# Kernel optimization log

Hardware: AMD Instinct MI355X
Metric: run time of the kernel (lower is better)

The kernel has to match this reference:

```python
import jax, jax.numpy as jnp
import numpy as np

N = 20000          # num_nodes
E = 160000         # directed edges (doubled to undirected inside reference)
NF, EF, H, OUT, K = 16, 16, 128, 16, 3


def mlp2(x, w1, b1, w2, b2):
    return jnp.maximum(x @ w1 + b1, 0.0) @ w2 + b2


def edge_agg(x, src, dst, eattr, w1, b1, w2, b2):
    # message = MLP(cat[x_i (target), x_j (source), edge_attr]); aggr='add' at target
    m = mlp2(jnp.concatenate([x[dst], x[src], eattr], axis=-1), w1, b1, w2, b2)
    return jax.ops.segment_sum(m, dst, num_segments=x.shape[0])


def tag_conv(x, src, dst, lins, bias):
    # PyG TAGConv: gcn_norm (no self loops), out = sum_k lin_k(L^k x) + bias
    n = x.shape[0]
    deg = jax.ops.segment_sum(jnp.ones_like(src, dtype=x.dtype), dst, num_segments=n)
    dis = jnp.where(deg > 0, jax.lax.rsqrt(deg), 0.0)
    norm = dis[src] * dis[dst]                     # [E]
    out = x @ lins[0]
    h = x
    for k in range(1, lins.shape[0]):
        h = jax.ops.segment_sum(norm[:, None] * h[src], dst, num_segments=n)
        out = out + h @ lins[k]
    return out + bias


def setup_inputs() -> dict:
    key = jax.random.key(0)
    ks = jax.random.split(key, 20)
    s = 0.05
    lin = lambda k, i, o: jax.random.normal(k, (i, o), jnp.float32) * s
    inp = {}
    inp["x"] = jax.random.normal(ks[0], (N, NF), jnp.float32)
    inp["mask"] = (jax.random.uniform(ks[1], (N, NF)) > 0.5).astype(jnp.float32)
    inp["edge_attr"] = jax.random.normal(ks[2], (E, EF), jnp.float32)
    inp["edge_index"] = jax.random.randint(ks[3], (2, E), 0, N)
    inp["m_w1"] = lin(ks[4], NF, H); inp["m_b1"] = jnp.zeros(H)
    inp["m_w2"] = lin(ks[5], H, NF); inp["m_b2"] = jnp.zeros(NF)
    inp["ea0_w1"] = lin(ks[6], 2 * NF + EF, H); inp["ea0_b1"] = jnp.zeros(H)
    inp["ea0_w2"] = lin(ks[7], H, H); inp["ea0_b2"] = jnp.zeros(H)
    inp["tag0_w"] = jax.random.normal(ks[8], (K + 1, H, H), jnp.float32) * s
    inp["tag0_b"] = jnp.zeros(H)
    inp["ea1_w1"] = lin(ks[9], 2 * H + EF, H); inp["ea1_b1"] = jnp.zeros(H)
    inp["ea1_w2"] = lin(ks[10], H, H); inp["ea1_b2"] = jnp.zeros(H)
    inp["tag1_w"] = jax.random.normal(ks[11], (K + 1, H, H), jnp.float32) * s
    inp["tag1_b"] = jnp.zeros(H)
    inp["ea2_w1"] = lin(ks[12], 2 * H + EF, H); inp["ea2_b1"] = jnp.zeros(H)
    inp["ea2_w2"] = lin(ks[13], H, OUT); inp["ea2_b2"] = jnp.zeros(OUT)
    return inp


def reference(x, mask, edge_attr, m_w1, m_b1, m_w2, m_b2,
              ea0_w1, ea0_b1, ea0_w2, ea0_b2, tag0_w, tag0_b,
              ea1_w1, ea1_b1, ea1_w2, ea1_b2, tag1_w, tag1_b,
              ea2_w1, ea2_b1, ea2_w2, ea2_b2, edge_index):
    # undirect_graph: random directed edges -> duplicate reversed copies
    src0, dst0 = edge_index[0], edge_index[1]
    src = jnp.concatenate([src0, dst0])
    dst = jnp.concatenate([dst0, src0])
    ea = jnp.concatenate([edge_attr, edge_attr], axis=0)
    # mask embedding + residual
    h = mlp2(mask, m_w1, m_b1, m_w2, m_b2) + x
    # [EA, TAG, EA, TAG] with ReLU (dropout = identity in eval)
    h = jnp.maximum(edge_agg(h, src, dst, ea, ea0_w1, ea0_b1, ea0_w2, ea0_b2), 0.0)
    h = jnp.maximum(tag_conv(h, src, dst, tag0_w, tag0_b), 0.0)
    h = jnp.maximum(edge_agg(h, src, dst, ea, ea1_w1, ea1_b1, ea1_w2, ea1_b2), 0.0)
    h = jnp.maximum(tag_conv(h, src, dst, tag1_w, tag1_b), 0.0)
    # final EA (no activation)
    return edge_agg(h, src, dst, ea, ea2_w1, ea2_b1, ea2_w2, ea2_b2)
```

## Files before the change

kernel.cpp:

```cpp
#include <hip/hip_runtime.h>

typedef unsigned short u16;
typedef unsigned int u32;

using bfrag  = __attribute__((ext_vector_type(8))) short;
using f32x4  = __attribute__((ext_vector_type(4))) float;
using f32x16 = __attribute__((ext_vector_type(16))) float;

__device__ __forceinline__ float b2f(u16 u) {
  union { u32 i; float f; } c; c.i = ((u32)u) << 16; return c.f;
}
__device__ __forceinline__ float bflo(u32 u) { union { u32 i; float f; } c; c.i = u << 16; return c.f; }
__device__ __forceinline__ float bfhi(u32 u) { union { u32 i; float f; } c; c.i = u & 0xffff0000u; return c.f; }
__device__ __forceinline__ u16 f2b(float f) {
  union { float f; u32 i; } c; c.f = f;
  u32 x = c.i;
  u32 r = x + 0x7fffu + ((x >> 16) & 1u);
  return (u16)(r >> 16);
}
__device__ __forceinline__ u32 packb2(float x, float y) {
  return ((u32)f2b(x)) | (((u32)f2b(y)) << 16);
}
__device__ __forceinline__ u16 f2h(float x) {
  union { _Float16 h; u16 u; } c; c.h = (_Float16)x; return c.u;
}
__device__ __forceinline__ float h2lo(u32 u) { union { u32 i; _Float16 h[2]; } c; c.i = u; return (float)c.h[0]; }
__device__ __forceinline__ float h2hi(u32 u) { union { u32 i; _Float16 h[2]; } c; c.i = u; return (float)c.h[1]; }
__device__ __forceinline__ int rfl(int v) { return __builtin_amdgcn_readfirstlane(v); }

__global__ __launch_bounds__(256) void prologue(
    const float* __restrict__ ea, const int* __restrict__ eidx,
    const float* __restrict__ ea0_w1, const float* __restrict__ ea0_w2,
    const float* __restrict__ tag0_w, const float* __restrict__ ea1_w1,
    const float* __restrict__ ea1_w2, const float* __restrict__ tag1_w,
    const float* __restrict__ ea2_w1,
    u16* __restrict__ P0, u16* __restrict__ P1, u16* __restrict__ P2,
    int* __restrict__ degi, u16* __restrict__ Wt, int E, int N,
    int PB, int CB) {
  int t = threadIdx.x;
  if (blockIdx.x < (unsigned)PB) {
    __shared__ u16 Alds[64 * 16];
    __shared__ u16 Wlds[3 * 2048];
    int base = blockIdx.x * 64;
    int rows = E - base; if (rows > 64) rows = 64;
    const float* wsrc[3] = { ea0_w1 + 32 * 128, ea1_w1 + 256 * 128, ea2_w1 + 256 * 128 };
#pragma unroll
    for (int i = 0; i < 8; ++i) {
      int idx = i * 256 + t;
      int n = idx >> 4, k = idx & 15;
      Wlds[0 * 2048 + idx] = f2b(wsrc[0][k * 128 + n]);
      Wlds[1 * 2048 + idx] = f2b(wsrc[1][k * 128 + n]);
      Wlds[2 * 2048 + idx] = f2b(wsrc[2][k * 128 + n]);
    }
#pragma unroll
    for (int i = 0; i < 4; ++i) {
      int idx = (i * 256 + t) * 4;
      float4 v = make_float4(0.f, 0.f, 0.f, 0.f);
      if ((idx >> 4) < rows) v = *(const float4*)(ea + (size_t)base * 16 + idx);
      ushort4 h;
      h.x = f2b(v.x); h.y = f2b(v.y); h.z = f2b(v.z); h.w = f2b(v.w);
      *(ushort4*)(Alds + idx) = h;
    }
    __syncthreads();
    int wave = t >> 6, lane = t & 63;
    int rowt = (wave >> 1) * 32;
    int colt = (wave & 1) * 64;
    int mm = lane & 31, kh = lane >> 5;
    bfrag a = *(const bfrag*)(Alds + (rowt + mm) * 16 + kh * 8);
#pragma unroll
    for (int tab = 0; tab < 3; ++tab) {
      const u16* wl = Wlds + tab * 2048;
      bfrag b0 = *(const bfrag*)(wl + (colt + 2 * mm) * 16 + kh * 8);
      bfrag b1 = *(const bfrag*)(wl + (colt + 2 * mm + 1) * 16 + kh * 8);
      f32x16 acc0, acc1;
#pragma unroll
      for (int z = 0; z < 16; ++z) { acc0[z] = 0.f; acc1[z] = 0.f; }
      acc0 = __builtin_amdgcn_mfma_f32_32x32x16_bf16(a, b0, acc0, 0, 0, 0);
      acc1 = __builtin_amdgcn_mfma_f32_32x32x16_bf16(a, b1, acc1, 0, 0, 0);
      u16* P = (tab == 0) ? P0 : (tab == 1) ? P1 : P2;
#pragma unroll
      for (int reg = 0; reg < 16; ++reg) {
        int row = rowt + (reg & 3) + 8 * (reg >> 2) + 4 * kh;
        if (row < rows) {
          u32 pr = ((u32)f2h(acc0[reg])) | (((u32)f2h(acc1[reg])) << 16);
          *(u32*)(P + (size_t)(base + row) * 128 + colt + 2 * mm) = pr;
        }
      }
    }
    return;
  }
  if (blockIdx.x < (unsigned)(PB + CB)) {
    int e = (blockIdx.x - PB) * 256 + t;
    if (e < E) {
      atomicAdd(&degi[eidx[E + e]], 1);
      atomicAdd(&degi[eidx[e]], 1);
    }
    return;
  }
  int wb = blockIdx.x - PB - CB;
  int mat = wb >> 3, chunk = wb & 7;
  const float* src;
  if      (mat == 0)  src = ea0_w2;
  else if (mat <= 4)  src = tag0_w + (mat - 1) * 16384;
  else if (mat == 5)  src = ea1_w1;
  else if (mat == 6)  src = ea1_w1 + 16384;
  else if (mat == 7)  src = ea1_w2;
  else if (mat <= 11) src = tag1_w + (mat - 8) * 16384;
  else if (mat == 12) src = ea2_w1;
  else                src = ea2_w1 + 16384;
  u16* dst = Wt + mat * 16384;
  for (int i = 0; i < 8; ++i) {
    int idx = chunk * 2048 + i * 256 + t;
    int k = idx >> 7, n = idx & 127;
    dst[n * 128 + k] = f2b(src[idx]);
  }
}

__global__ __launch_bounds__(256) void scan1(const int* __restrict__ degi,
                                             int* __restrict__ bsum, int N) {
  __shared__ int sh[256];
  int t = threadIdx.x;
  int gid = blockIdx.x * 256 + t;
  sh[t] = (gid < N) ? degi[gid] : 0;
  __syncthreads();
  for (int off = 128; off > 0; off >>= 1) {
    if (t < off) sh[t] += sh[t + off];
    __syncthreads();
  }
  if (t == 0) bsum[blockIdx.x] = sh[0];
}

__global__ __launch_bounds__(256) void scan2(int* __restrict__ bsum,
                                             int* __restrict__ rowptr, int nb, int N) {
  __shared__ int sh[256];
  int t = threadIdx.x;
  int v = (t < nb) ? bsum[t] : 0;
  sh[t] = v;
  __syncthreads();
  for (int off = 1; off < 256; off <<= 1) {
    int x = sh[t];
    int add = (t >= off) ? sh[t - off] : 0;
    __syncthreads();
    sh[t] = x + add;
    __syncthreads();
  }
  if (t < nb) bsum[t] = sh[t] - v;
  if (t == nb - 1) rowptr[N] = sh[t];
}

__global__ __launch_bounds__(256) void scan3(const int* __restrict__ degi,
                                             const int* __restrict__ bsum,
                                             int* __restrict__ rowptr,
                                             int* __restrict__ cursor,
                                             float* __restrict__ dis, int N) {
  __shared__ int sh[256];
  int t = threadIdx.x;
  int gid = blockIdx.x * 256 + t;
  int d = (gid < N) ? degi[gid] : 0;
  sh[t] = d;
  __syncthreads();
  for (int off = 1; off < 256; off <<= 1) {
    int x = sh[t];
    int add = (t >= off) ? sh[t - off] : 0;
    __syncthreads();
    sh[t] = x + add;
    __syncthreads();
  }
  if (gid < N) {
    int run = bsum[blockIdx.x] + sh[t] - d;
    rowptr[gid] = run;
    cursor[gid] = run;
    dis[gid] = d > 0 ? rsqrtf((float)d) : 0.0f;
  }
}

__global__ __launch_bounds__(256) void fill_head(
    const int* __restrict__ eidx, int* __restrict__ cursor,
    const float* __restrict__ dis, int2* __restrict__ cw, int2* __restrict__ ce, int E,
    const float* __restrict__ mask, const float* __restrict__ x,
    const float* __restrict__ m_w1, const float* __restrict__ m_b1,
    const float* __restrict__ m_w2, const float* __restrict__ m_b2,
    const float* __restrict__ ea0_w1, const float* __restrict__ ea0_b1,
    u16* __restrict__ pb, u16* __restrict__ q, int M, int FB) {
  int t = threadIdx.x;
  if (blockIdx.x < (unsigned)FB) {
    int i = blockIdx.x * 256 + t;
    int E2 = 2 * E;
    if (i >= E2) return;
    int e = (i < E) ? i : i - E;
    int s, d;
    if (i < E) { s = eidx[e]; d = eidx[E + e]; }
    else       { s = eidx[E + e]; d = eidx[e]; }
    int pos = atomicAdd(&cursor[d], 1);
    cw[pos] = make_int2(s, __float_as_int(dis[s]));
    ce[pos] = make_int2(s, e);
    return;
  }
  __shared__ float Ml[16 * 16];
  __shared__ float T1[16 * 128];
  __shared__ float H[16 * 16];
  int base = (blockIdx.x - FB) * 16;
  {
    int r = t >> 4, k = t & 15;
    int row = base + r;
    Ml[t] = (row < M) ? mask[(size_t)row * 16 + k] : 0.f;
  }
  __syncthreads();
  {
    int col = t & 127, h2 = t >> 7;
    float acc[8];
    float b1v = m_b1[col];
#pragma unroll
    for (int r = 0; r < 8; ++r) acc[r] = b1v;
    for (int k = 0; k < 16; ++k) {
      float w = m_w1[k * 128 + col];
#pragma unroll
      for (int r = 0; r < 8; ++r) acc[r] += Ml[(h2 * 8 + r) * 16 + k] * w;
    }
#pragma unroll
    for (int r = 0; r < 8; ++r) T1[(h2 * 8 + r) * 128 + col] = fmaxf(acc[r], 0.f);
  }
  __syncthreads();
  {
    int r = t >> 4, u = t & 15;
    float acc = m_b2[u];
    for (int k = 0; k < 128; ++k) acc += T1[r * 128 + k] * m_w2[k * 16 + u];
    int row = base + r;
    float xv = (row < M) ? x[(size_t)row * 16 + u] : 0.f;
    H[t] = acc + xv;
  }
  __syncthreads();
  {
    int col = t & 127, h2 = t >> 7;
    float aP[8], aQ[8];
    float b1v = ea0_b1[col];
#pragma unroll
    for (int r = 0; r < 8; ++r) { aP[r] = b1v; aQ[r] = 0.f; }
    for (int k = 0; k < 16; ++k) {
      float wd = ea0_w1[k * 128 + col];
      float ws = ea0_w1[(16 + k) * 128 + col];
#pragma unroll
      for (int r = 0; r < 8; ++r) {
        float h = H[(h2 * 8 + r) * 16 + k];
        aP[r] += h * wd;
        aQ[r] += h * ws;
      }
    }
#pragma unroll
    for (int r = 0; r < 8; ++r) {
      int row = base + h2 * 8 + r;
      if (row < M) {
        pb[(size_t)row * 128 + col] = f2b(aP[r]);
        q[(size_t)row * 128 + col]  = f2b(aQ[r]);
      }
    }
  }
}

__global__ __launch_bounds__(256) void gemm_mfma_dual(
    const u16* __restrict__ A, const u16* __restrict__ W0t, const u16* __restrict__ W1t,
    u16* __restrict__ C0, u16* __restrict__ C1, const float* __restrict__ bias0, int M) {
  __shared__ u16 Alds[64 * 136];
  __shared__ u16 Wlds[128 * 136];
  int t = threadIdx.x;
  int base = blockIdx.x * 64;
#pragma unroll
  for (int i = 0; i < 8; ++i) {
    int idx = (i * 256 + t) * 8;
    int n = idx >> 7, k = idx & 127;
    uint4 v = *(const uint4*)(W0t + idx);
    *(uint4*)(Wlds + n * 136 + k) = v;
  }
#pragma unroll
  for (int i = 0; i < 4; ++i) {
    int idx = (i * 256 + t) * 8;
    int r = idx >> 7, k = idx & 127;
    int row = base + r;
    uint4 v = make_uint4(0, 0, 0, 0);
    if (row < M) v = *(const uint4*)(A + (size_t)row * 128 + k);
    *(uint4*)(Alds + r * 136 + k) = v;
  }
  __syncthreads();
  int wave = t >> 6, lane = t & 63;
  int m = lane & 15, quad = lane >> 4;
  int arow = wave * 16 + m;
  bfrag a[4];
#pragma unroll
  for (int ks = 0; ks < 4; ++ks)
    a[ks] = *(const bfrag*)(Alds + arow * 136 + ks * 32 + quad * 8);
  f32x4 acc0[8], acc1[8];
#pragma unroll
  for (int nt = 0; nt < 8; ++nt) { acc0[nt] = (f32x4){0,0,0,0}; acc1[nt] = (f32x4){0,0,0,0}; }
#pragma unroll
  for (int nt = 0; nt < 8; ++nt) {
    int n = nt * 16 + m;
#pragma unroll
    for (int ks = 0; ks < 4; ++ks) {
      bfrag b = *(const bfrag*)(Wlds + n * 136 + ks * 32 + quad * 8);
      acc0[nt] = __builtin_amdgcn_mfma_f32_16x16x32_bf16(a[ks], b, acc0[nt], 0, 0, 0);
    }
  }
  __syncthreads();
#pragma unroll
  for (int i = 0; i < 8; ++i) {
    int idx = (i * 256 + t) * 8;
    int n = idx >> 7, k = idx & 127;
    uint4 v = *(const uint4*)(W1t + idx);
    *(uint4*)(Wlds + n * 136 + k) = v;
  }
  __syncthreads();
#pragma unroll
  for (int nt = 0; nt < 8; ++nt) {
    int n = nt * 16 + m;
#pragma unroll
    for (int ks = 0; ks < 4; ++ks) {
      bfrag b = *(const bfrag*)(Wlds + n * 136 + ks * 32 + quad * 8);
      acc1[nt] = __builtin_amdgcn_mfma_f32_16x16x32_bf16(a[ks], b, acc1[nt], 0, 0, 0);
    }
  }
#pragma unroll
  for (int nt = 0; nt < 8; ++nt) {
    int col = nt * 16 + m;
#pragma unroll
    for (int r = 0; r < 4; ++r) {
      int row = base + wave * 16 + quad * 4 + r;
      if (row < M) {
        float v0 = acc0[nt][r];
        if (bias0) v0 += bias0[col];
        C0[(size_t)row * 128 + col] = f2b(v0);
        C1[(size_t)row * 128 + col] = f2b(acc1[nt][r]);
      }
    }
  }
}

__global__ __launch_bounds__(256) void gemm_mfma_penta(
    const u16* __restrict__ A, const u16* __restrict__ W2t, const u16* __restrict__ Wt4,
    const float* __restrict__ bias, const int* __restrict__ degi,
    u16* __restrict__ G0, u16* __restrict__ G1,
    u16* __restrict__ G2, u16* __restrict__ G3, int M) {
  __shared__ u16 Alds[64 * 136];
  __shared__ u16 Wlds[128 * 136];
  int t = threadIdx.x;
  int base = blockIdx.x * 64;
#pragma unroll
  for (int i = 0; i < 8; ++i) {
    int idx = (i * 256 + t) * 8;
    int n = idx >> 7, k = idx & 127;
    uint4 v = *(const uint4*)(W2t + idx);
    *(uint4*)(Wlds + n * 136 + k) = v;
  }
#pragma unroll
  for (int i = 0; i < 4; ++i) {
    int idx = (i * 256 + t) * 8;
    int r = idx >> 7, k = idx & 127;
    int row = base + r;
    uint4 v = make_uint4(0, 0, 0, 0);
    if (row < M) v = *(const uint4*)(A + (size_t)row * 128 + k);
    *(uint4*)(Alds + r * 136 + k) = v;
  }
  __syncthreads();
  int wave = t >> 6, lane = t & 63;
  int m = lane & 15, quad = lane >> 4;
  int arow = wave * 16 + m;
  bfrag a[4];
#pragma unroll
  for (int ks = 0; ks < 4; ++ks)
    a[ks] = *(const bfrag*)(Alds + arow * 136 + ks * 32 + quad * 8);
  {
    f32x4 acc[8];
#pragma unroll
    for (int nt = 0; nt < 8; ++nt) acc[nt] = (f32x4){0.f, 0.f, 0.f, 0.f};
#pragma unroll
    for (int nt = 0; nt < 8; ++nt) {
      int n = nt * 16 + m;
#pragma unroll
      for (int ks = 0; ks < 4; ++ks) {
        bfrag b = *(const bfrag*)(Wlds + n * 136 + ks * 32 + quad * 8);
        acc[nt] = __builtin_amdgcn_mfma_f32_16x16x32_bf16(a[ks], b, acc[nt], 0, 0, 0);
      }
    }
#pragma unroll
    for (int nt = 0; nt < 8; ++nt) {
      int col = nt * 16 + m;
#pragma unroll
      for (int r = 0; r < 4; ++r) {
        int lrow = wave * 16 + quad * 4 + r;
        int row = base + lrow;
        float v = 0.f;
        if (row < M) v = fmaxf(acc[nt][r] + bias[col] * (float)degi[row], 0.f);
        Alds[lrow * 136 + col] = f2b(v);
      }
    }
  }
#pragma unroll
  for (int ks = 0; ks < 4; ++ks)
    a[ks] = *(const bfrag*)(Alds + arow * 136 + ks * 32 + quad * 8);
#pragma unroll
  for (int mat = 0; mat < 4; ++mat) {
    __syncthreads();
#pragma unroll
    for (int i = 0; i < 8; ++i) {
      int idx = (i * 256 + t) * 8;
      int n = idx >> 7, k = idx & 127;
      uint4 v = *(const uint4*)(Wt4 + mat * 16384 + idx);
      *(uint4*)(Wlds + n * 136 + k) = v;
    }
    __syncthreads();
    f32x4 acc[8];
#pragma unroll
    for (int nt = 0; nt < 8; ++nt) acc[nt] = (f32x4){0.f, 0.f, 0.f, 0.f};
#pragma unroll
    for (int nt = 0; nt < 8; ++nt) {
      int n = nt * 16 + m;
#pragma unroll
      for (int ks = 0; ks < 4; ++ks) {
        bfrag b = *(const bfrag*)(Wlds + n * 136 + ks * 32 + quad * 8);
        acc[nt] = __builtin_amdgcn_mfma_f32_16x16x32_bf16(a[ks], b, acc[nt], 0, 0, 0);
      }
    }
    u16* G = (mat == 0) ? G0 : (mat == 1) ? G1 : (mat == 2) ? G2 : G3;
#pragma unroll
    for (int nt = 0; nt < 8; ++nt) {
      int col = nt * 16 + m;
#pragma unroll
      for (int r = 0; r < 4; ++r) {
        int row = base + wave * 16 + quad * 4 + r;
        if (row < M) G[(size_t)row * 128 + col] = f2b(acc[nt][r]);
      }
    }
  }
}

__global__ __launch_bounds__(128) void gemm_tail(
    const u16* __restrict__ A, const float* __restrict__ W, float* __restrict__ Cout,
    const float* __restrict__ bias, const int* __restrict__ degi, int M) {
  const int ROWS = 8;
  int t = threadIdx.x;
  int base = blockIdx.x * ROWS;
  __shared__ float Al[ROWS * 128];
  for (int i = t; i < ROWS * 128; i += 128) {
    int r = i >> 7, k = i & 127;
    int row = base + r;
    Al[i] = (row < M) ? b2f(A[(size_t)row * 128 + k]) : 0.f;
  }
  __syncthreads();
  int r = t >> 4, u = t & 15;
  int row = base + r;
  float acc = 0.f;
  for (int k = 0; k < 128; ++k) acc += Al[r * 128 + k] * W[k * 16 + u];
  if (row < M) {
    Cout[(size_t)row * 16 + u] = acc + bias[u] * (float)degi[row];
  }
}

__device__ __forceinline__ void tag_edge(const int2* __restrict__ rr, int j,
    const u16* __restrict__ g, int lane, float& x0, float& x1) {
  int2 r = rr[j];
  int s = rfl(r.x); float w = __uint_as_float(rfl(r.y));
  u32 h = *((const u32*)(g + (size_t)s * 128) + lane);
  x0 += w * bflo(h); x1 += w * bfhi(h);
}
__device__ __forceinline__ void ea_edge(const int2* __restrict__ rr, int j,
    const u16* __restrict__ q, const u16* __restrict__ P, int lane,
    float pb0, float pb1, float& x0, float& x1) {
  int2 r = rr[j];
  int s = rfl(r.x), i = rfl(r.y);
  u32 qv = *((const u32*)(q + (size_t)s * 128) + lane);
  u32 pv = *((const u32*)(P + (size_t)i * 128) + lane);
  x0 += fmaxf(pb0 + bflo(qv) + h2lo(pv), 0.f);
  x1 += fmaxf(pb1 + bfhi(qv) + h2hi(pv), 0.f);
}

template<bool FINAL>
__global__ __launch_bounds__(256) void tag_gather8(
    const u16* __restrict__ g, const u16* __restrict__ Cin,
    const float* __restrict__ bias, const float* __restrict__ dis,
    const int* __restrict__ rowptr, const int2* __restrict__ cw,
    u16* __restrict__ out, int N) {
  __shared__ int2 recs[4][64];
  int wave = threadIdx.x >> 6, lane = threadIdx.x & 63;
  int node = blockIdx.x * 4 + wave;
  if (node >= N) return;
  int e0 = rfl(rowptr[node]);
  int e1 = rfl(rowptr[node + 1]);
  int2* rr = recs[wave];
  float a0 = 0, a1 = 0, b0 = 0, b1 = 0;
  for (int base = e0; base < e1; base += 64) {
    if (base + lane < e1) rr[lane] = cw[base + lane];
    int cnt = min(64, e1 - base);
    int j = 0;
    for (; j + 8 <= cnt; j += 8) {
      tag_edge(rr, j + 0, g, lane, a0, a1);
      tag_edge(rr, j + 1, g, lane, b0, b1);
      tag_edge(rr, j + 2, g, lane, a0, a1);
      tag_edge(rr, j + 3, g, lane, b0, b1);
      tag_edge(rr, j + 4, g, lane, a0, a1);
      tag_edge(rr, j + 5, g, lane, b0, b1);
      tag_edge(rr, j + 6, g, lane, a0, a1);
      tag_edge(rr, j + 7, g, lane, b0, b1);
    }
    for (; j + 2 <= cnt; j += 2) {
      tag_edge(rr, j + 0, g, lane, a0, a1);
      tag_edge(rr, j + 1, g, lane, b0, b1);
    }
    if (j < cnt) tag_edge(rr, j, g, lane, a0, a1);
  }
  float dn = dis[node];
  float r0v = dn * (a0 + b0), r1v = dn * (a1 + b1);
  u32 cin = *((const u32*)(Cin + (size_t)node * 128) + lane);
  r0v += bflo(cin); r1v += bfhi(cin);
  if (FINAL) {
    float2 bv = *(const float2*)(bias + 2 * lane);
    r0v = fmaxf(r0v + bv.x, 0.f);
    r1v = fmaxf(r1v + bv.y, 0.f);
  }
  *((u32*)(out + (size_t)node * 128) + lane) = packb2(r0v, r1v);
}

__global__ __launch_bounds__(256) void ea_gather8(
    const u16* __restrict__ pb, const u16* __restrict__ q,
    const u16* __restrict__ P ,
    const int* __restrict__ rowptr, const int2* __restrict__ ce,
    u16* __restrict__ Hsum, int N) {
  __shared__ int2 recs[4][64];
  int wave = threadIdx.x >> 6, lane = threadIdx.x & 63;
  int node = blockIdx.x * 4 + wave;
  if (node >= N) return;
  int e0 = rfl(rowptr[node]);
  int e1 = rfl(rowptr[node + 1]);
  int2* rr = recs[wave];
  u32 pbu = *((const u32*)(pb + (size_t)node * 128) + lane);
  float pb0 = bflo(pbu), pb1 = bfhi(pbu);
  float a0 = 0, a1 = 0, b0 = 0, b1 = 0;
  for (int base = e0; base < e1; base += 64) {
    if (base + lane < e1) rr[lane] = ce[base + lane];
    int cnt = min(64, e1 - base);
    int j = 0;
    for (; j + 8 <= cnt; j += 8) {
      ea_edge(rr, j + 0, q, P, lane, pb0, pb1, a0, a1);
      ea_edge(rr, j + 1, q, P, lane, pb0, pb1, b0, b1);
      ea_edge(rr, j + 2, q, P, lane, pb0, pb1, a0, a1);
      ea_edge(rr, j + 3, q, P, lane, pb0, pb1, b0, b1);
      ea_edge(rr, j + 4, q, P, lane, pb0, pb1, a0, a1);
      ea_edge(rr, j + 5, q, P, lane, pb0, pb1, b0, b1);
      ea_edge(rr, j + 6, q, P, lane, pb0, pb1, a0, a1);
      ea_edge(rr, j + 7, q, P, lane, pb0, pb1, b0, b1);
    }
    for (; j + 2 <= cnt; j += 2) {
      ea_edge(rr, j + 0, q, P, lane, pb0, pb1, a0, a1);
      ea_edge(rr, j + 1, q, P, lane, pb0, pb1, b0, b1);
    }
    if (j < cnt) ea_edge(rr, j, q, P, lane, pb0, pb1, a0, a1);
  }
  *((u32*)(Hsum + (size_t)node * 128) + lane) = packb2(a0 + b0, a1 + b1);
}

extern "C" void kernel_launch(void* const* d_in, const int* in_sizes, int n_in,
                              void* d_out, int out_size, void* d_ws, size_t ws_size,
                              hipStream_t stream) {
  const float* x      = (const float*)d_in[0];
  const float* mask   = (const float*)d_in[1];
  const float* ea     = (const float*)d_in[2];
  const int*   eidx   = (const int*)d_in[3];
  const float* m_w1   = (const float*)d_in[4];
  const float* m_b1   = (const float*)d_in[5];
  const float* m_w2   = (const float*)d_in[6];
  const float* m_b2   = (const float*)d_in[7];
  const float* ea0_w1 = (const float*)d_in[8];
  const float* ea0_b1 = (const float*)d_in[9];
  const float* ea0_w2 = (const float*)d_in[10];
  const float* ea0_b2 = (const float*)d_in[11];
  const float* tag0_w = (const float*)d_in[12];
  const float* tag0_b = (const float*)d_in[13];
  const float* ea1_w1 = (const float*)d_in[14];
  const float* ea1_b1 = (const float*)d_in[15];
  const float* ea1_w2 = (const float*)d_in[16];
  const float* ea1_b2 = (const float*)d_in[17];
  const float* tag1_w = (const float*)d_in[18];
  const float* tag1_b = (const float*)d_in[19];
  const float* ea2_w1 = (const float*)d_in[20];
  const float* ea2_b1 = (const float*)d_in[21];
  const float* ea2_w2 = (const float*)d_in[22];
  const float* ea2_b2 = (const float*)d_in[23];

  const int N = in_sizes[0] / 16;
  const int E = in_sizes[2] / 16;
  const int E2 = 2 * E;
  const int NB = (N + 255) / 256;

  char* w = (char*)d_ws;
  auto alloc = [&](size_t bytes) { char* p = w; w += (bytes + 255) & ~(size_t)255; return p; };
  int*   degi   = (int*)alloc((size_t)N * 4);
  int*   cursor = (int*)alloc((size_t)N * 4);
  int*   rowptr = (int*)alloc((size_t)(N + 1) * 4);
  int*   bsum   = (int*)alloc((size_t)256 * 4);
  float* dis    = (float*)alloc((size_t)N * 4);
  int2*  cw     = (int2*)alloc((size_t)E2 * 8);
  int2*  ce     = (int2*)alloc((size_t)E2 * 8);
  u16*   X0     = (u16*)alloc((size_t)N * 128 * 2);
  u16*   X1     = (u16*)alloc((size_t)N * 128 * 2);
  u16*   X2     = (u16*)alloc((size_t)N * 128 * 2);
  u16*   G0     = (u16*)alloc((size_t)N * 128 * 2);
  u16*   G1     = (u16*)alloc((size_t)N * 128 * 2);
  u16*   G2     = (u16*)alloc((size_t)N * 128 * 2);
  u16*   G3     = (u16*)alloc((size_t)N * 128 * 2);
  u16*   Wt     = (u16*)alloc((size_t)14 * 16384 * 2);
  u16*   P0     = (u16*)alloc((size_t)E * 128 * 2);
  u16*   P1     = (u16*)alloc((size_t)E * 128 * 2);
  u16*   P2     = (u16*)alloc((size_t)E * 128 * 2);
  (void)ws_size; (void)n_in; (void)out_size;

  const int PB = (E + 63) / 64;
  const int CB = (E + 255) / 256;
  const int FB = (E2 + 255) / 256;
  const int HB = (N + 15) / 16;
  const int gm = (N + 63) / 64;
  const int g4 = (N + 3) / 4;
  const int gb = (N + 7) / 8;

  u16* WT_ea0w2  = Wt + 0 * 16384;
  u16* WT_tag0   = Wt + 1 * 16384;
  u16* WT_ea1d   = Wt + 5 * 16384;
  u16* WT_ea1s   = Wt + 6 * 16384;
  u16* WT_ea1w2  = Wt + 7 * 16384;
  u16* WT_tag1   = Wt + 8 * 16384;
  u16* WT_ea2d   = Wt + 12 * 16384;
  u16* WT_ea2s   = Wt + 13 * 16384;

  hipMemsetAsync(degi, 0, (size_t)N * 4, stream);
  prologue<<<PB + CB + 112, 256, 0, stream>>>(ea, eidx, ea0_w1, ea0_w2, tag0_w,
                                              ea1_w1, ea1_w2, tag1_w, ea2_w1,
                                              P0, P1, P2, degi, Wt, E, N, PB, CB);
  scan1<<<NB, 256, 0, stream>>>(degi, bsum, N);
  scan2<<<1, 256, 0, stream>>>(bsum, rowptr, NB, N);
  scan3<<<NB, 256, 0, stream>>>(degi, bsum, rowptr, cursor, dis, N);
  fill_head<<<FB + HB, 256, 0, stream>>>(eidx, cursor, dis, cw, ce, E,
                                         mask, x, m_w1, m_b1, m_w2, m_b2,
                                         ea0_w1, ea0_b1, X0, X1, N, FB);

  ea_gather8<<<g4, 256, 0, stream>>>(X0, X1, P0, rowptr, ce, X2, N);
  gemm_mfma_penta<<<gm, 256, 0, stream>>>(X2, WT_ea0w2, WT_tag0, ea0_b2, degi,
                                          G0, G1, G2, G3, N);
  tag_gather8<false><<<g4, 256, 0, stream>>>(G3, G2, nullptr, dis, rowptr, cw, X1, N);
  tag_gather8<false><<<g4, 256, 0, stream>>>(X1, G1, nullptr, dis, rowptr, cw, X2, N);
  tag_gather8<true><<<g4, 256, 0, stream>>>(X2, G0, tag0_b, dis, rowptr, cw, X0, N);

  gemm_mfma_dual<<<gm, 256, 0, stream>>>(X0, WT_ea1d, WT_ea1s, X1, X2, ea1_b1, N);
  ea_gather8<<<g4, 256, 0, stream>>>(X1, X2, P1, rowptr, ce, G0, N);
  gemm_mfma_penta<<<gm, 256, 0, stream>>>(G0, WT_ea1w2, WT_tag1, ea1_b2, degi,
                                          G0, G1, G2, G3, N);
  tag_gather8<false><<<g4, 256, 0, stream>>>(G3, G2, nullptr, dis, rowptr, cw, X1, N);
  tag_gather8<false><<<g4, 256, 0, stream>>>(X1, G1, nullptr, dis, rowptr, cw, X2, N);
  tag_gather8<true><<<g4, 256, 0, stream>>>(X2, G0, tag1_b, dis, rowptr, cw, X0, N);

  gemm_mfma_dual<<<gm, 256, 0, stream>>>(X0, WT_ea2d, WT_ea2s, X1, X2, ea2_b1, N);
  ea_gather8<<<g4, 256, 0, stream>>>(X1, X2, P2, rowptr, ce, G0, N);
  gemm_tail<<<gb, 128, 0, stream>>>(G0, ea2_w2, (float*)d_out, ea2_b2, degi, N);
}
```

Baseline: 421.8 us.

## Merge CSR edge records, fuse scan2/scan3, restructure edge-attr projection blocks

Merges the two per-edge CSR record arrays (source+weight and source+edge id) into one 16-byte int4 record, written once in fill_head and shared by all gather kernels. Fuses the single-block scan2 into scan3: every block now redoes the small block-sum scan itself, which removes one launch. Reorganises the edge-attribute projection prologue so each block handles 256 edges for a single weight table instead of 64 edges for all three tables. The cost is a wider record that every gather kernel loads per edge, 16 bytes where each previously read 8.

```diff
diff --git a/kernel.cpp b/kernel.cpp
--- a/kernel.cpp
+++ b/kernel.cpp
@@ -36,21 +36,24 @@
     const float* __restrict__ ea2_w1,
     u16* __restrict__ P0, u16* __restrict__ P1, u16* __restrict__ P2,
     int* __restrict__ degi, u16* __restrict__ Wt, int E, int N,
-    int PB, int CB) {
+    int PB, int CB, int EB) {
   int t = threadIdx.x;
   if (blockIdx.x < (unsigned)PB) {
-    __shared__ u16 Alds[64 * 16];
-    __shared__ u16 Wlds[3 * 2048];
-    int base = blockIdx.x * 64;
-    int rows = E - base; if (rows > 64) rows = 64;
-    const float* wsrc[3] = { ea0_w1 + 32 * 128, ea1_w1 + 256 * 128, ea2_w1 + 256 * 128 };
+    __shared__ u16 Alds[256 * 16];
+    __shared__ u16 Wlds[2048];
+    int tab = blockIdx.x / EB;
+    int chunk = blockIdx.x - tab * EB;
+    int base = chunk * 256;
+    int rows = E - base; if (rows > 256) rows = 256;
+    const float* wsrc = (tab == 0) ? (ea0_w1 + 32 * 128)
+                      : (tab == 1) ? (ea1_w1 + 256 * 128)
+                                   : (ea2_w1 + 256 * 128);
+    u16* P = (tab == 0) ? P0 : (tab == 1) ? P1 : P2;
 #pragma unroll
     for (int i = 0; i < 8; ++i) {
       int idx = i * 256 + t;
       int n = idx >> 4, k = idx & 15;
-      Wlds[0 * 2048 + idx] = f2b(wsrc[0][k * 128 + n]);
-      Wlds[1 * 2048 + idx] = f2b(wsrc[1][k * 128 + n]);
-      Wlds[2 * 2048 + idx] = f2b(wsrc[2][k * 128 + n]);
+      Wlds[idx] = f2b(wsrc[k * 128 + n]);
     }
 #pragma unroll
     for (int i = 0; i < 4; ++i) {
@@ -63,21 +66,23 @@
     }
     __syncthreads();
     int wave = t >> 6, lane = t & 63;
-    int rowt = (wave >> 1) * 32;
-    int colt = (wave & 1) * 64;
     int mm = lane & 31, kh = lane >> 5;
-    bfrag a = *(const bfrag*)(Alds + (rowt + mm) * 16 + kh * 8);
-#pragma unroll
-    for (int tab = 0; tab < 3; ++tab) {
-      const u16* wl = Wlds + tab * 2048;
-      bfrag b0 = *(const bfrag*)(wl + (colt + 2 * mm) * 16 + kh * 8);
-      bfrag b1 = *(const bfrag*)(wl + (colt + 2 * mm + 1) * 16 + kh * 8);
+    bfrag b00 = *(const bfrag*)(Wlds + (2 * mm) * 16 + kh * 8);
+    bfrag b01 = *(const bfrag*)(Wlds + (2 * mm + 1) * 16 + kh * 8);
+    bfrag b10 = *(const bfrag*)(Wlds + (64 + 2 * mm) * 16 + kh * 8);
+    bfrag b11 = *(const bfrag*)(Wlds + (64 + 2 * mm + 1) * 16 + kh * 8);
+#pragma unroll
+    for (int it = 0; it < 4; ++it) {
+      int task = wave + it * 4;
+      int rowt = (task >> 1) * 32;
+      int ch = task & 1;
+      int colt = ch * 64;
+      bfrag a = *(const bfrag*)(Alds + (rowt + mm) * 16 + kh * 8);
       f32x16 acc0, acc1;
 #pragma unroll
       for (int z = 0; z < 16; ++z) { acc0[z] = 0.f; acc1[z] = 0.f; }
-      acc0 = __builtin_amdgcn_mfma_f32_32x32x16_bf16(a, b0, acc0, 0, 0, 0);
-      acc1 = __builtin_amdgcn_mfma_f32_32x32x16_bf16(a, b1, acc1, 0, 0, 0);
-      u16* P = (tab == 0) ? P0 : (tab == 1) ? P1 : P2;
+      acc0 = __builtin_amdgcn_mfma_f32_32x32x16_bf16(a, ch ? b10 : b00, acc0, 0, 0, 0);
+      acc1 = __builtin_amdgcn_mfma_f32_32x32x16_bf16(a, ch ? b11 : b01, acc1, 0, 0, 0);
 #pragma unroll
       for (int reg = 0; reg < 16; ++reg) {
         int row = rowt + (reg & 3) + 8 * (reg >> 2) + 4 * kh;
@@ -130,8 +135,11 @@
   if (t == 0) bsum[blockIdx.x] = sh[0];
 }
 
-__global__ __launch_bounds__(256) void scan2(int* __restrict__ bsum,
-                                             int* __restrict__ rowptr, int nb, int N) {
+__global__ __launch_bounds__(256) void scan23(const int* __restrict__ degi,
+                                              const int* __restrict__ bsum,
+                                              int* __restrict__ rowptr,
+                                              int* __restrict__ cursor,
+                                              float* __restrict__ dis, int nb, int N) {
   __shared__ int sh[256];
   int t = threadIdx.x;
   int v = (t < nb) ? bsum[t] : 0;
@@ -144,17 +152,9 @@
     sh[t] = x + add;
     __syncthreads();
   }
-  if (t < nb) bsum[t] = sh[t] - v;
-  if (t == nb - 1) rowptr[N] = sh[t];
-}
-
-__global__ __launch_bounds__(256) void scan3(const int* __restrict__ degi,
-                                             const int* __restrict__ bsum,
-                                             int* __restrict__ rowptr,
-                                             int* __restrict__ cursor,
-                                             float* __restrict__ dis, int N) {
-  __shared__ int sh[256];
-  int t = threadIdx.x;
+  int blockoff = (blockIdx.x == 0) ? 0 : sh[blockIdx.x - 1];
+  int total = sh[nb - 1];
+  __syncthreads();
   int gid = blockIdx.x * 256 + t;
   int d = (gid < N) ? degi[gid] : 0;
   sh[t] = d;
@@ -167,16 +167,17 @@
     __syncthreads();
   }
   if (gid < N) {
-    int run = bsum[blockIdx.x] + sh[t] - d;
+    int run = blockoff + sh[t] - d;
     rowptr[gid] = run;
     cursor[gid] = run;
     dis[gid] = d > 0 ? rsqrtf((float)d) : 0.0f;
   }
+  if (blockIdx.x == 0 && t == 0) rowptr[N] = total;
 }
 
 __global__ __launch_bounds__(256) void fill_head(
     const int* __restrict__ eidx, int* __restrict__ cursor,
-    const float* __restrict__ dis, int2* __restrict__ cw, int2* __restrict__ ce, int E,
+    const float* __restrict__ dis, int4* __restrict__ cr, int E,
     const float* __restrict__ mask, const float* __restrict__ x,
     const float* __restrict__ m_w1, const float* __restrict__ m_b1,
     const float* __restrict__ m_w2, const float* __restrict__ m_b2,
@@ -192,8 +193,7 @@
     if (i < E) { s = eidx[e]; d = eidx[E + e]; }
     else       { s = eidx[E + e]; d = eidx[e]; }
     int pos = atomicAdd(&cursor[d], 1);
-    cw[pos] = make_int2(s, __float_as_int(dis[s]));
-    ce[pos] = make_int2(s, e);
+    cr[pos] = make_int4(s, e, __float_as_int(dis[s]), 0);
     return;
   }
   __shared__ float Ml[16 * 16];
@@ -454,17 +454,17 @@
   }
 }
 
-__device__ __forceinline__ void tag_edge(const int2* __restrict__ rr, int j,
+__device__ __forceinline__ void tag_edge(const int4* __restrict__ rr, int j,
     const u16* __restrict__ g, int lane, float& x0, float& x1) {
-  int2 r = rr[j];
-  int s = rfl(r.x); float w = __uint_as_float(rfl(r.y));
+  int4 r = rr[j];
+  int s = rfl(r.x); float w = __uint_as_float(rfl(r.z));
   u32 h = *((const u32*)(g + (size_t)s * 128) + lane);
   x0 += w * bflo(h); x1 += w * bfhi(h);
 }
-__device__ __forceinline__ void ea_edge(const int2* __restrict__ rr, int j,
+__device__ __forceinline__ void ea_edge(const int4* __restrict__ rr, int j,
     const u16* __restrict__ q, const u16* __restrict__ P, int lane,
     float pb0, float pb1, float& x0, float& x1) {
-  int2 r = rr[j];
+  int4 r = rr[j];
   int s = rfl(r.x), i = rfl(r.y);
   u32 qv = *((const u32*)(q + (size_t)s * 128) + lane);
   u32 pv = *((const u32*)(P + (size_t)i * 128) + lane);
@@ -473,21 +473,21 @@
 }
 
 template<bool FINAL>
-__global__ __launch_bounds__(256) void tag_gather8(
+__global__ __launch_bounds__(256) void tag_gather9(
     const u16* __restrict__ g, const u16* __restrict__ Cin,
     const float* __restrict__ bias, const float* __restrict__ dis,
-    const int* __restrict__ rowptr, const int2* __restrict__ cw,
+    const int* __restrict__ rowptr, const int4* __restrict__ cr,
     u16* __restrict__ out, int N) {
-  __shared__ int2 recs[4][64];
+  __shared__ int4 recs[4][64];
   int wave = threadIdx.x >> 6, lane = threadIdx.x & 63;
   int node = blockIdx.x * 4 + wave;
   if (node >= N) return;
   int e0 = rfl(rowptr[node]);
   int e1 = rfl(rowptr[node + 1]);
-  int2* rr = recs[wave];
+  int4* rr = recs[wave];
   float a0 = 0, a1 = 0, b0 = 0, b1 = 0;
   for (int base = e0; base < e1; base += 64) {
-    if (base + lane < e1) rr[lane] = cw[base + lane];
+    if (base + lane < e1) rr[lane] = cr[base + lane];
     int cnt = min(64, e1 - base);
     int j = 0;
     for (; j + 8 <= cnt; j += 8) {
@@ -518,23 +518,23 @@
   *((u32*)(out + (size_t)node * 128) + lane) = packb2(r0v, r1v);
 }
 
-__global__ __launch_bounds__(256) void ea_gather8(
+__global__ __launch_bounds__(256) void ea_gather9(
     const u16* __restrict__ pb, const u16* __restrict__ q,
     const u16* __restrict__ P ,
-    const int* __restrict__ rowptr, const int2* __restrict__ ce,
+    const int* __restrict__ rowptr, const int4* __restrict__ cr,
     u16* __restrict__ Hsum, int N) {
-  __shared__ int2 recs[4][64];
+  __shared__ int4 recs[4][64];
   int wave = threadIdx.x >> 6, lane = threadIdx.x & 63;
   int node = blockIdx.x * 4 + wave;
   if (node >= N) return;
   int e0 = rfl(rowptr[node]);
   int e1 = rfl(rowptr[node + 1]);
-  int2* rr = recs[wave];
+  int4* rr = recs[wave];
   u32 pbu = *((const u32*)(pb + (size_t)node * 128) + lane);
   float pb0 = bflo(pbu), pb1 = bfhi(pbu);
   float a0 = 0, a1 = 0, b0 = 0, b1 = 0;
   for (int base = e0; base < e1; base += 64) {
-    if (base + lane < e1) rr[lane] = ce[base + lane];
+    if (base + lane < e1) rr[lane] = cr[base + lane];
     int cnt = min(64, e1 - base);
     int j = 0;
     for (; j + 8 <= cnt; j += 8) {
@@ -596,8 +596,7 @@
   int*   rowptr = (int*)alloc((size_t)(N + 1) * 4);
   int*   bsum   = (int*)alloc((size_t)256 * 4);
   float* dis    = (float*)alloc((size_t)N * 4);
-  int2*  cw     = (int2*)alloc((size_t)E2 * 8);
-  int2*  ce     = (int2*)alloc((size_t)E2 * 8);
+  int4*  cr     = (int4*)alloc((size_t)E2 * 16);
   u16*   X0     = (u16*)alloc((size_t)N * 128 * 2);
   u16*   X1     = (u16*)alloc((size_t)N * 128 * 2);
   u16*   X2     = (u16*)alloc((size_t)N * 128 * 2);
@@ -611,7 +610,8 @@
   u16*   P2     = (u16*)alloc((size_t)E * 128 * 2);
   (void)ws_size; (void)n_in; (void)out_size;
 
-  const int PB = (E + 63) / 64;
+  const int EB = (E + 255) / 256;
+  const int PB = 3 * EB;
   const int CB = (E + 255) / 256;
   const int FB = (E2 + 255) / 256;
   const int HB = (N + 15) / 16;
@@ -631,30 +631,29 @@
   hipMemsetAsync(degi, 0, (size_t)N * 4, stream);
   prologue<<<PB + CB + 112, 256, 0, stream>>>(ea, eidx, ea0_w1, ea0_w2, tag0_w,
                                               ea1_w1, ea1_w2, tag1_w, ea2_w1,
-                                              P0, P1, P2, degi, Wt, E, N, PB, CB);
+                                              P0, P1, P2, degi, Wt, E, N, PB, CB, EB);
   scan1<<<NB, 256, 0, stream>>>(degi, bsum, N);
-  scan2<<<1, 256, 0, stream>>>(bsum, rowptr, NB, N);
-  scan3<<<NB, 256, 0, stream>>>(degi, bsum, rowptr, cursor, dis, N);
-  fill_head<<<FB + HB, 256, 0, stream>>>(eidx, cursor, dis, cw, ce, E,
+  scan23<<<NB, 256, 0, stream>>>(degi, bsum, rowptr, cursor, dis, NB, N);
+  fill_head<<<FB + HB, 256, 0, stream>>>(eidx, cursor, dis, cr, E,
                                          mask, x, m_w1, m_b1, m_w2, m_b2,
                                          ea0_w1, ea0_b1, X0, X1, N, FB);
 
-  ea_gather8<<<g4, 256, 0, stream>>>(X0, X1, P0, rowptr, ce, X2, N);
+  ea_gather9<<<g4, 256, 0, stream>>>(X0, X1, P0, rowptr, cr, X2, N);
   gemm_mfma_penta<<<gm, 256, 0, stream>>>(X2, WT_ea0w2, WT_tag0, ea0_b2, degi,
                                           G0, G1, G2, G3, N);
-  tag_gather8<false><<<g4, 256, 0, stream>>>(G3, G2, nullptr, dis, rowptr, cw, X1, N);
-  tag_gather8<false><<<g4, 256, 0, stream>>>(X1, G1, nullptr, dis, rowptr, cw, X2, N);
-  tag_gather8<true><<<g4, 256, 0, stream>>>(X2, G0, tag0_b, dis, rowptr, cw, X0, N);
+  tag_gather9<false><<<g4, 256, 0, stream>>>(G3, G2, nullptr, dis, rowptr, cr, X1, N);
+  tag_gather9<false><<<g4, 256, 0, stream>>>(X1, G1, nullptr, dis, rowptr, cr, X2, N);
+  tag_gather9<true><<<g4, 256, 0, stream>>>(X2, G0, tag0_b, dis, rowptr, cr, X0, N);
 
   gemm_mfma_dual<<<gm, 256, 0, stream>>>(X0, WT_ea1d, WT_ea1s, X1, X2, ea1_b1, N);
-  ea_gather8<<<g4, 256, 0, stream>>>(X1, X2, P1, rowptr, ce, G0, N);
+  ea_gather9<<<g4, 256, 0, stream>>>(X1, X2, P1, rowptr, cr, G0, N);
   gemm_mfma_penta<<<gm, 256, 0, stream>>>(G0, WT_ea1w2, WT_tag1, ea1_b2, degi,
                                           G0, G1, G2, G3, N);
-  tag_gather8<false><<<g4, 256, 0, stream>>>(G3, G2, nullptr, dis, rowptr, cw, X1, N);
-  tag_gather8<false><<<g4, 256, 0, stream>>>(X1, G1, nullptr, dis, rowptr, cw, X2, N);
-  tag_gather8<true><<<g4, 256, 0, stream>>>(X2, G0, tag1_b, dis, rowptr, cw, X0, N);
+  tag_gather9<false><<<g4, 256, 0, stream>>>(G3, G2, nullptr, dis, rowptr, cr, X1, N);
+  tag_gather9<false><<<g4, 256, 0, stream>>>(X1, G1, nullptr, dis, rowptr, cr, X2, N);
+  tag_gather9<true><<<g4, 256, 0, stream>>>(X2, G0, tag1_b, dis, rowptr, cr, X0, N);
 
   gemm_mfma_dual<<<gm, 256, 0, stream>>>(X0, WT_ea2d, WT_ea2s, X1, X2, ea2_b1, N);
-  ea_gather8<<<g4, 256, 0, stream>>>(X1, X2, P2, rowptr, ce, G0, N);
+  ea_gather9<<<g4, 256, 0, stream>>>(X1, X2, P2, rowptr, cr, G0, N);
   gemm_tail<<<gb, 128, 0, stream>>>(G0, ea2_w2, (float*)d_out, ea2_b2, degi, N);
 }
```

Result: faster. 413.2 us (-2.0%).
